# Kernel tuning notes

Measured on AMD Instinct MI355X. Metric: run time of the kernel, lower is better.

## Reference

```python
import jax, jax.numpy as jnp
import numpy as np

B, S, D_MODEL, FFN, P = 8, 4096, 256, 1024, 8
BLK = 256  # token block size for the max-plus reduction


def setup_inputs() -> dict:
    key = jax.random.key(0)
    ks = jax.random.split(key, 12)
    x = jax.random.normal(ks[0], (B, S, D_MODEL), jnp.float32)
    # TropicalLinear params (additive semiring weights -> small scale)
    Wt = 0.05 * jax.random.normal(ks[1], (FFN, D_MODEL), jnp.float32)
    bt = 0.05 * jax.random.normal(ks[2], (FFN,), jnp.float32)
    # LFDualActivation: per-channel piecewise-linear convex (max) and concave (min)
    # branches, blended by a per-channel sigmoid gate alpha ('blend' mode).
    sl_cvx = 1.0 + 0.1 * jax.random.normal(ks[3], (FFN, P), jnp.float32)
    of_cvx = 0.1 * jax.random.normal(ks[4], (FFN, P), jnp.float32)
    sl_ccv = 1.0 + 0.1 * jax.random.normal(ks[5], (FFN, P), jnp.float32)
    of_ccv = 0.1 * jax.random.normal(ks[6], (FFN, P), jnp.float32)
    alpha = jnp.zeros((FFN,), jnp.float32)
    # Classical branch
    Wc = jax.random.normal(ks[7], (D_MODEL, FFN), jnp.float32) / np.sqrt(D_MODEL)
    bc = jnp.zeros((FFN,), jnp.float32)
    # Gate: init per source (weight ~0, bias +2.0 -> g ~ 0.88 tropical)
    Wg = 0.01 * jax.random.normal(ks[8], (D_MODEL, FFN), jnp.float32)
    bg = 2.0 * jnp.ones((FFN,), jnp.float32)
    # Down projection
    Wd = jax.random.normal(ks[9], (FFN, D_MODEL), jnp.float32) / np.sqrt(FFN)
    bd = jnp.zeros((D_MODEL,), jnp.float32)
    return {"x": x, "Wt": Wt, "bt": bt, "sl_cvx": sl_cvx, "of_cvx": of_cvx,
            "sl_ccv": sl_ccv, "of_ccv": of_ccv, "alpha": alpha,
            "Wc": Wc, "bc": bc, "Wg": Wg, "bg": bg, "Wd": Wd, "bd": bd}


def reference(x, Wt, bt, sl_cvx, of_cvx, sl_ccv, of_ccv, alpha, Wc, bc, Wg, bg, Wd, bd):
    Bx, Sx, D = x.shape
    T = Bx * Sx
    xf = x.reshape(T, D)
    xb = xf.reshape(T // BLK, BLK, D)
    s = jax.nn.sigmoid(alpha)  # [FFN]

    def blk_fn(xx):  # xx: [BLK, D]
        # Tropical (max-plus) linear: t[n,m] = max_k(xx[n,k] + Wt[m,k]) + bt[m]
        t = jnp.max(xx[:, None, :] + Wt[None, :, :], axis=-1) + bt  # [BLK, FFN]
        # LF dual activation: blend of convex (max of lines) and concave (min of lines)
        z = t[:, :, None]  # [BLK, FFN, 1]
        cvx = jnp.max(z * sl_cvx[None] + of_cvx[None], axis=-1)
        ccv = jnp.min(z * sl_ccv[None] + of_ccv[None], axis=-1)
        return s * cvx + (1.0 - s) * ccv  # [BLK, FFN]

    trop = jax.lax.map(blk_fn, xb).reshape(T, FFN)  # dropout = identity (eval)
    classical = jax.nn.gelu(xf @ Wc + bc, approximate=False)
    g = jax.nn.sigmoid(xf @ Wg + bg)
    fused = g * trop + (1.0 - g) * classical
    out = fused @ Wd + bd  # final dropout = identity (eval)
    return out.reshape(Bx, Sx, D)
```

## Files before the change

### kernel.cpp

```cpp
#include <hip/hip_runtime.h>

#define TTOK 32768
#define DM   256
#define NF   1024
#define KMAX 32

typedef __attribute__((ext_vector_type(8))) unsigned short ushort8;
typedef __attribute__((ext_vector_type(8))) __bf16 bf16x8;
typedef __attribute__((ext_vector_type(4))) float floatx4;

constexpr size_t O_SLOT = 0;
constexpr size_t O_S    = 256;
constexpr size_t O_WCT  = O_S    + 4096;
constexpr size_t O_WGT  = O_WCT  + (size_t)NF*DM*2;
constexpr size_t O_WDT  = O_WGT  + (size_t)NF*DM*2;
constexpr size_t O_WTT  = O_WDT  + (size_t)DM*NF*2;
constexpr size_t O_XBF  = O_WTT  + (size_t)DM*NF*4;
constexpr size_t O_CNT  = O_XBF  + (size_t)TTOK*DM*2;
constexpr size_t O_CIDX = O_CNT  + (size_t)TTOK*4;
constexpr size_t O_CVAL = O_CIDX + (size_t)TTOK*KMAX*4;
constexpr size_t O_FUSD = O_CVAL + (size_t)TTOK*KMAX*4;

__device__ __forceinline__ float bf2f(unsigned short u) {
    union { unsigned int i; float f; } c; c.i = ((unsigned int)u) << 16; return c.f;
}
__device__ __forceinline__ unsigned short f2bf(float v) {
    union { float f; unsigned int i; } c; c.f = v;
    unsigned int b = c.i;
    return (unsigned short)((b + 0x7FFFu + ((b >> 16) & 1u)) >> 16);
}
__device__ __forceinline__ float sigm(float z) { return 1.0f / (1.0f + __expf(-z)); }
__device__ __forceinline__ float gelu_f(float x) {
    return x * sigm(1.59576912f * (x + 0.044715f * x * x * x));
}
__device__ __forceinline__ void g2lds16(const unsigned short* g, unsigned short* l) {
    __builtin_amdgcn_global_load_lds((const __attribute__((address_space(1))) unsigned int*)g,
                                     (__attribute__((address_space(3))) unsigned int*)l, 16, 0, 0);
}

__global__ void pack_kernel(const float* __restrict__ Wt, const float* __restrict__ alpha,
                            const float* __restrict__ Wc, const float* __restrict__ Wg,
                            const float* __restrict__ Wd,
                            unsigned short* __restrict__ Wct, unsigned short* __restrict__ Wgt,
                            unsigned short* __restrict__ WdT, float* __restrict__ WtT,
                            float* __restrict__ s, unsigned int* __restrict__ slot) {
    int e = blockIdx.x * 256 + threadIdx.x;
    if (e == 0) *slot = 0u;
    { int f = e >> 8, k = e & 255;
      Wct[e] = f2bf(Wc[k * NF + f]);
      Wgt[e] = f2bf(Wg[k * NF + f]); }
    { int n = e >> 10, k = e & 1023;
      WdT[e] = f2bf(Wd[k * DM + n]); }
    { int d = e >> 10, f = e & 1023;
      WtT[e] = Wt[f * DM + d]; }
    if (e < NF) s[e] = sigm(alpha[e]);
}

__global__ void minmax_kernel(const float* __restrict__ Wt, unsigned int* __restrict__ slot) {
    int g = blockIdx.x * 256 + threadIdx.x;
    float lm = 0.0f;
    for (int i = g; i < NF * DM; i += 128 * 256) lm = fmaxf(lm, fabsf(Wt[i]));
    #pragma unroll
    for (int o = 32; o > 0; o >>= 1) lm = fmaxf(lm, __shfl_xor(lm, o));
    if ((threadIdx.x & 63) == 0) atomicMax(slot, __float_as_uint(lm));
}

__global__ __launch_bounds__(256) void cand_kernel(
        const float* __restrict__ x, const unsigned int* __restrict__ slot,
        unsigned short* __restrict__ xbf, int* __restrict__ counts,
        int* __restrict__ cidx, float* __restrict__ cval) {
    const int wave = threadIdx.x >> 6, lane = threadIdx.x & 63;
    const int tok = blockIdx.x * 4 + wave;
    const float* xr = x + (size_t)tok * DM;
    float v0 = xr[lane], v1 = xr[lane + 64], v2 = xr[lane + 128], v3 = xr[lane + 192];
    unsigned short* xo = xbf + (size_t)tok * DM;
    xo[lane]       = f2bf(v0);
    xo[lane + 64]  = f2bf(v1);
    xo[lane + 128] = f2bf(v2);
    xo[lane + 192] = f2bf(v3);
    float m = fmaxf(fmaxf(v0, v1), fmaxf(v2, v3));
    #pragma unroll
    for (int o = 32; o > 0; o >>= 1) m = fmaxf(m, __shfl_xor(m, o));
    const float delta = 2.0f * __uint_as_float(*slot);
    const float thr = m - delta;
    const unsigned long long lt = (lane == 63) ? 0x7FFFFFFFFFFFFFFFull
                                               : ((1ull << lane) - 1ull);
    float vv[4] = { v0, v1, v2, v3 };
    int base = 0;
    #pragma unroll
    for (int j = 0; j < 4; j++) {
        bool p = vv[j] >= thr;
        unsigned long long mask = __ballot(p);
        int pos = base + __popcll(mask & lt);
        if (p && pos < KMAX) {
            cidx[(size_t)tok * KMAX + pos] = lane + j * 64;
            cval[(size_t)tok * KMAX + pos] = vv[j];
        }
        base += __popcll(mask);
    }
    if (lane == 0) counts[tok] = base;
}

#define LDSS  32
#define KCAP  16
#define KPADL 17
#define OSTR  136
#define STAGEB 24576
__global__ __launch_bounds__(512, 4) void gemm1_kernel(
    const unsigned short* __restrict__ A,
    const unsigned short* __restrict__ Bct,
    const unsigned short* __restrict__ Bgt,
    const float* __restrict__ bc, const float* __restrict__ bg,
    const int* __restrict__ counts, const int* __restrict__ cidx,
    const float* __restrict__ cval, const float* __restrict__ x,
    const float* __restrict__ WtT, const float* __restrict__ bt,
    const float* __restrict__ slx, const float* __restrict__ ofx,
    const float* __restrict__ slc, const float* __restrict__ ofc,
    const float* __restrict__ s, unsigned short* __restrict__ fused) {
    __shared__ __align__(16) char smem[76800];
    unsigned short* obuf = (unsigned short*)smem;
    float* par = (float*)(smem + 49152);
    int* sOV  = (int*)(smem + 67584);
    int* sCnt = (int*)(smem + 76288);
    const int t = threadIdx.x;
    const int b = blockIdx.x;
    const int xcd = b & 7, j = b >> 3;
    const int bf = j & 7;
    const int bm = (j >> 3) * 8 + xcd;
    const int wave = t >> 6, lane = t & 63;
    const int wm = wave & 1, wn = wave >> 1;
    const int lr = lane & 15, quad = lane >> 4;
    const int srow = wave * 16 + (lane >> 2), scol = (lane & 3) << 3;
    const unsigned short* gA = A   + (size_t)(bm * 128 + srow) * DM + scol;
    const unsigned short* gC = Bct + (size_t)(bf * 128 + srow) * DM + scol;
    const unsigned short* gG = Bgt + (size_t)(bf * 128 + srow) * DM + scol;
    const int lofs = wave * 16 * LDSS;

    if (t < 128) sCnt[t] = counts[bm * 128 + t];
    const int PADV = (int)(((unsigned int)f2bf(-1e30f)) << 16);
    #pragma unroll
    for (int e = t; e < 2048; e += 512) {
        int m = e >> 4, k = e & 15;
        int c = counts[bm * 128 + m];
        int pk = PADV;
        if (k < (c < KCAP ? c : KCAP)) {
            int d  = cidx[(size_t)(bm * 128 + m) * KMAX + k];
            float v = cval[(size_t)(bm * 128 + m) * KMAX + k];
            pk = (int)(((unsigned int)f2bf(v)) << 16) | d;
        }
        sOV[m * KPADL + k] = pk;
    }
    #pragma unroll
    for (int e = t; e < 1024; e += 512) {
        int ff = e >> 3, w = e & 7;
        int gf = (bf * 128 + ff) * 8 + w;
        par[ff * 36 + w]      = slx[gf];
        par[ff * 36 + 8 + w]  = ofx[gf];
        par[ff * 36 + 16 + w] = slc[gf];
        par[ff * 36 + 24 + w] = ofc[gf];
    }
    if (t < 128) {
        int gf = bf * 128 + t;
        par[t * 36 + 32] = bt[gf];
        par[t * 36 + 33] = s[gf];
        par[t * 36 + 34] = bc[gf];
        par[t * 36 + 35] = bg[gf];
    }

    floatx4 accc[4][2], accg[4][2];
    #pragma unroll
    for (int i = 0; i < 4; i++)
        #pragma unroll
        for (int jj = 0; jj < 2; jj++) { accc[i][jj] = (floatx4)0.0f; accg[i][jj] = (floatx4)0.0f; }

    {
        unsigned short* b0 = (unsigned short*)smem;
        g2lds16(gA, b0 + lofs);
        g2lds16(gC, b0 + 4096 + lofs);
        g2lds16(gG, b0 + 8192 + lofs);
    }
    __syncthreads();
    #pragma unroll
    for (int k = 0; k < 8; k++) {
        unsigned short* cur = (unsigned short*)(smem + (size_t)(k & 1) * STAGEB);
        if (k < 7) {
            unsigned short* nxt = (unsigned short*)(smem + (size_t)((k + 1) & 1) * STAGEB);
            int k0 = (k + 1) * 32;
            g2lds16(gA + k0, nxt + lofs);
            g2lds16(gC + k0, nxt + 4096 + lofs);
            g2lds16(gG + k0, nxt + 8192 + lofs);
        }
        bf16x8 af[4], bcf[2], bgf[2];
        #pragma unroll
        for (int mi = 0; mi < 4; mi++)
            af[mi] = *(const bf16x8*)&cur[(wm * 64 + mi * 16 + lr) * LDSS + quad * 8];
        #pragma unroll
        for (int ni = 0; ni < 2; ni++) {
            bcf[ni] = *(const bf16x8*)&cur[4096 + (wn * 32 + ni * 16 + lr) * LDSS + quad * 8];
            bgf[ni] = *(const bf16x8*)&cur[8192 + (wn * 32 + ni * 16 + lr) * LDSS + quad * 8];
        }
        #pragma unroll
        for (int mi = 0; mi < 4; mi++)
            #pragma unroll
            for (int ni = 0; ni < 2; ni++) {
                accc[mi][ni] = __builtin_amdgcn_mfma_f32_16x16x32_bf16(af[mi], bcf[ni], accc[mi][ni], 0, 0, 0);
                accg[mi][ni] = __builtin_amdgcn_mfma_f32_16x16x32_bf16(af[mi], bgf[ni], accg[mi][ni], 0, 0, 0);
            }
        __syncthreads();
    }

    const int f0 = bf * 128 + wn * 32 + lr;
    #pragma unroll
    for (int mi = 0; mi < 4; mi++) {
        const int mb = wm * 64 + mi * 16 + quad * 4;
        int c0 = sCnt[mb], c1 = sCnt[mb + 1], c2 = sCnt[mb + 2], c3 = sCnt[mb + 3];
        int k0c = c0 < KCAP ? c0 : KCAP, k1c = c1 < KCAP ? c1 : KCAP;
        int k2c = c2 < KCAP ? c2 : KCAP, k3c = c3 < KCAP ? c3 : KCAP;
        int km = max(max(k0c, k1c), max(k2c, k3c));
        float z0a = -1e30f, z1a = -1e30f, z2a = -1e30f, z3a = -1e30f;
        float z0b = -1e30f, z1b = -1e30f, z2b = -1e30f, z3b = -1e30f;
        for (int k = 0; k < km; k++) {
            int p0 = sOV[(mb + 0) * KPADL + k];
            int p1 = sOV[(mb + 1) * KPADL + k];
            int p2 = sOV[(mb + 2) * KPADL + k];
            int p3 = sOV[(mb + 3) * KPADL + k];
            const float* r0 = WtT + ((p0 & 0xFFFF) << 10) + f0;
            const float* r1 = WtT + ((p1 & 0xFFFF) << 10) + f0;
            const float* r2 = WtT + ((p2 & 0xFFFF) << 10) + f0;
            const float* r3 = WtT + ((p3 & 0xFFFF) << 10) + f0;
            float w0a = r0[0], w0b = r0[16];
            float w1a = r1[0], w1b = r1[16];
            float w2a = r2[0], w2b = r2[16];
            float w3a = r3[0], w3b = r3[16];
            float v0 = __int_as_float(p0 & 0xFFFF0000);
            float v1 = __int_as_float(p1 & 0xFFFF0000);
            float v2 = __int_as_float(p2 & 0xFFFF0000);
            float v3 = __int_as_float(p3 & 0xFFFF0000);
            z0a = fmaxf(z0a, v0 + w0a); z0b = fmaxf(z0b, v0 + w0b);
            z1a = fmaxf(z1a, v1 + w1a); z1b = fmaxf(z1b, v1 + w1b);
            z2a = fmaxf(z2a, v2 + w2a); z2b = fmaxf(z2b, v2 + w2b);
            z3a = fmaxf(z3a, v3 + w3a); z3b = fmaxf(z3b, v3 + w3b);
        }
        if (c0 > KCAP || c1 > KCAP || c2 > KCAP || c3 > KCAP) {
            float za[4] = { z0a, z1a, z2a, z3a };
            float zb[4] = { z0b, z1b, z2b, z3b };
            int cc[4] = { c0, c1, c2, c3 };
            #pragma unroll 1
            for (int r = 0; r < 4; r++) if (cc[r] > KCAP) {
                const float* xr = x + (size_t)(bm * 128 + mb + r) * DM;
                float ma = -1e30f, mbv = -1e30f;
                for (int d = 0; d < DM; d++) {
                    float xv = xr[d];
                    ma  = fmaxf(ma,  xv + WtT[d * NF + f0]);
                    mbv = fmaxf(mbv, xv + WtT[d * NF + f0 + 16]);
                }
                za[r] = ma; zb[r] = mbv;
            }
            z0a = za[0]; z1a = za[1]; z2a = za[2]; z3a = za[3];
            z0b = zb[0]; z1b = zb[1]; z2b = zb[2]; z3b = zb[3];
        }
        #pragma unroll
        for (int ni = 0; ni < 2; ni++) {
            const int fl = wn * 32 + ni * 16 + lr;
            const float* pp = par + fl * 36;
            float4 a0 = *(const float4*)(pp),      a1 = *(const float4*)(pp + 4);
            float4 b0 = *(const float4*)(pp + 8),  b1 = *(const float4*)(pp + 12);
            float4 cc0 = *(const float4*)(pp + 16), cc1 = *(const float4*)(pp + 20);
            float4 d0 = *(const float4*)(pp + 24), d1 = *(const float4*)(pp + 28);
            float4 sc = *(const float4*)(pp + 32);
            float zr[4];
            if (ni == 0) { zr[0] = z0a; zr[1] = z1a; zr[2] = z2a; zr[3] = z3a; }
            else         { zr[0] = z0b; zr[1] = z1b; zr[2] = z2b; zr[3] = z3b; }
            #pragma unroll
            for (int r = 0; r < 4; r++) {
                float z = zr[r] + sc.x;
                float cvx = fmaf(z, a0.x, b0.x);
                cvx = fmaxf(cvx, fmaf(z, a0.y, b0.y));
                cvx = fmaxf(cvx, fmaf(z, a0.z, b0.z));
                cvx = fmaxf(cvx, fmaf(z, a0.w, b0.w));
                cvx = fmaxf(cvx, fmaf(z, a1.x, b1.x));
                cvx = fmaxf(cvx, fmaf(z, a1.y, b1.y));
                cvx = fmaxf(cvx, fmaf(z, a1.z, b1.z));
                cvx = fmaxf(cvx, fmaf(z, a1.w, b1.w));
                float ccv = fmaf(z, cc0.x, d0.x);
                ccv = fminf(ccv, fmaf(z, cc0.y, d0.y));
                ccv = fminf(ccv, fmaf(z, cc0.z, d0.z));
                ccv = fminf(ccv, fmaf(z, cc0.w, d0.w));
                ccv = fminf(ccv, fmaf(z, cc1.x, d1.x));
                ccv = fminf(ccv, fmaf(z, cc1.y, d1.y));
                ccv = fminf(ccv, fmaf(z, cc1.z, d1.z));
                ccv = fminf(ccv, fmaf(z, cc1.w, d1.w));
                float tv = sc.y * cvx + (1.0f - sc.y) * ccv;
                float cpre = accc[mi][ni][r] + sc.z;
                float gpre = accg[mi][ni][r] + sc.w;
                float g = sigm(gpre);
                float cla = gelu_f(cpre);
                obuf[(mb + r) * OSTR + fl] = f2bf(g * tv + (1.0f - g) * cla);
            }
        }
    }
    __syncthreads();
    #pragma unroll
    for (int e = t; e < 128 * 16; e += 512) {
        int row = e >> 4, c8 = (e & 15) << 3;
        ushort8 v = *(const ushort8*)&obuf[row * OSTR + c8];
        *(ushort8*)&fused[(size_t)(bm * 128 + row) * NF + bf * 128 + c8] = v;
    }
}

#define LDS2 64
__global__ __launch_bounds__(512, 4) void gemm2_kernel(
    const unsigned short* __restrict__ A,
    const unsigned short* __restrict__ Bt,
    const float* __restrict__ bd, float* __restrict__ out) {
    __shared__ __align__(16) unsigned short As[128 * LDS2];
    __shared__ __align__(16) unsigned short Bs[128 * LDS2];
    const int t = threadIdx.x;
    const int b = blockIdx.x;
    const int xcd = b & 7, j = b >> 3;
    const int bn = j & 1;
    const int bm = (j >> 1) * 8 + xcd;
    const int wave = t >> 6, lane = t & 63;
    const int wm = wave & 1, wn = wave >> 1;
    const int lr = lane & 15, quad = lane >> 4;
    const int srow = wave * 8 + (lane >> 3), scol = (lane & 7) << 3;
    const unsigned short* gA = A  + (size_t)(bm * 128 + srow) * NF + scol;
    const unsigned short* gB = Bt + (size_t)(bn * 128 + srow) * NF + scol;
    unsigned short* lA = &As[wave * 8 * LDS2];
    unsigned short* lB = &Bs[wave * 8 * LDS2];

    floatx4 acc[4][2];
    #pragma unroll
    for (int i = 0; i < 4; i++)
        #pragma unroll
        for (int jj = 0; jj < 2; jj++) acc[i][jj] = (floatx4)0.0f;

    for (int k0 = 0; k0 < NF; k0 += 64) {
        __syncthreads();
        g2lds16(gA + k0, lA);
        g2lds16(gA + k0 + (size_t)64 * NF, lA + 64 * LDS2);
        g2lds16(gB + k0, lB);
        g2lds16(gB + k0 + (size_t)64 * NF, lB + 64 * LDS2);
        __syncthreads();
        #pragma unroll
        for (int ks = 0; ks < 2; ks++) {
            bf16x8 af[4], bf_[2];
            #pragma unroll
            for (int mi = 0; mi < 4; mi++)
                af[mi] = *(const bf16x8*)&As[(wm * 64 + mi * 16 + lr) * LDS2 + ks * 32 + quad * 8];
            #pragma unroll
            for (int ni = 0; ni < 2; ni++)
                bf_[ni] = *(const bf16x8*)&Bs[(wn * 32 + ni * 16 + lr) * LDS2 + ks * 32 + quad * 8];
            #pragma unroll
            for (int mi = 0; mi < 4; mi++)
                #pragma unroll
                for (int ni = 0; ni < 2; ni++)
                    acc[mi][ni] = __builtin_amdgcn_mfma_f32_16x16x32_bf16(af[mi], bf_[ni], acc[mi][ni], 0, 0, 0);
        }
    }
    #pragma unroll
    for (int mi = 0; mi < 4; mi++)
        #pragma unroll
        for (int ni = 0; ni < 2; ni++) {
            int n = bn * 128 + wn * 32 + ni * 16 + lr;
            float bdv = bd[n];
            #pragma unroll
            for (int r = 0; r < 4; r++) {
                int m = bm * 128 + wm * 64 + mi * 16 + quad * 4 + r;
                out[m * DM + n] = acc[mi][ni][r] + bdv;
            }
        }
}

extern "C" void kernel_launch(void* const* d_in, const int* in_sizes, int n_in,
                              void* d_out, int out_size, void* d_ws, size_t ws_size,
                              hipStream_t stream) {
    const float* x     = (const float*)d_in[0];
    const float* Wt    = (const float*)d_in[1];
    const float* bt    = (const float*)d_in[2];
    const float* slx   = (const float*)d_in[3];
    const float* ofx   = (const float*)d_in[4];
    const float* slc   = (const float*)d_in[5];
    const float* ofc   = (const float*)d_in[6];
    const float* alpha = (const float*)d_in[7];
    const float* Wc    = (const float*)d_in[8];
    const float* bc    = (const float*)d_in[9];
    const float* Wg    = (const float*)d_in[10];
    const float* bg    = (const float*)d_in[11];
    const float* Wd    = (const float*)d_in[12];
    const float* bd    = (const float*)d_in[13];
    float* out = (float*)d_out;
    char* ws = (char*)d_ws;

    unsigned int* slot = (unsigned int*)(ws + O_SLOT);
    float* s           = (float*)(ws + O_S);
    unsigned short* Wct = (unsigned short*)(ws + O_WCT);
    unsigned short* Wgt = (unsigned short*)(ws + O_WGT);
    unsigned short* WdT = (unsigned short*)(ws + O_WDT);
    float* WtT          = (float*)(ws + O_WTT);
    unsigned short* xbf = (unsigned short*)(ws + O_XBF);
    int* counts         = (int*)(ws + O_CNT);
    int* cidx           = (int*)(ws + O_CIDX);
    float* cval         = (float*)(ws + O_CVAL);
    unsigned short* fused = (unsigned short*)(ws + O_FUSD);

    pack_kernel<<<1024, 256, 0, stream>>>(Wt, alpha, Wc, Wg, Wd, Wct, Wgt, WdT, WtT, s, slot);
    minmax_kernel<<<128, 256, 0, stream>>>(Wt, slot);
    cand_kernel<<<TTOK / 4, 256, 0, stream>>>(x, slot, xbf, counts, cidx, cval);
    gemm1_kernel<<<2048, 512, 0, stream>>>(
        xbf, Wct, Wgt, bc, bg, counts, cidx, cval, x, WtT, bt,
        slx, ofx, slc, ofc, s, fused);
    gemm2_kernel<<<512, 512, 0, stream>>>(fused, WdT, bd, out);
}
```

Measured before the change: 328.5 us.

## Fuse Wt max into pack, defer gemm1 prologue, double-buffer gemm2, pack epilogue math

The separate minmax kernel is removed. Its |Wt| max reduction now runs inside pack_kernel, and the slot is zeroed with a memset. In gemm1, staging of candidates and activation parameters moves after the MFMA main loop so it no longer delays the first tile loads, and the final barrier is dropped. gemm2 moves from single-buffered LDS with two barriers per step to double-buffered prefetch. The max-plus gather and dual-activation epilogue are rewritten with 2-wide float vectors so the compiler can emit packed FMA/max/min. Together these cut a launch, overlap loads with MFMA, and reduce epilogue instruction count, at the cost of more LDS in gemm2 (which may lower occupancy).

```diff
diff --git a/kernel.cpp b/kernel.cpp
--- a/kernel.cpp
+++ b/kernel.cpp
@@ -8,6 +8,11 @@
 typedef __attribute__((ext_vector_type(8))) unsigned short ushort8;
 typedef __attribute__((ext_vector_type(8))) __bf16 bf16x8;
 typedef __attribute__((ext_vector_type(4))) float floatx4;
+typedef __attribute__((ext_vector_type(2))) float floatx2;
+
+#define PKFMA(a,b,c) __builtin_elementwise_fma(a,b,c)
+#define PKMAX(a,b)   __builtin_elementwise_max(a,b)
+#define PKMIN(a,b)   __builtin_elementwise_min(a,b)
 
 constexpr size_t O_SLOT = 0;
 constexpr size_t O_S    = 256;
@@ -45,24 +50,20 @@
                             unsigned short* __restrict__ WdT, float* __restrict__ WtT,
                             float* __restrict__ s, unsigned int* __restrict__ slot) {
     int e = blockIdx.x * 256 + threadIdx.x;
-    if (e == 0) *slot = 0u;
     { int f = e >> 8, k = e & 255;
       Wct[e] = f2bf(Wc[k * NF + f]);
       Wgt[e] = f2bf(Wg[k * NF + f]); }
     { int n = e >> 10, k = e & 1023;
       WdT[e] = f2bf(Wd[k * DM + n]); }
+    float wv;
     { int d = e >> 10, f = e & 1023;
-      WtT[e] = Wt[f * DM + d]; }
-    if (e < NF) s[e] = sigm(alpha[e]);
-}
-
-__global__ void minmax_kernel(const float* __restrict__ Wt, unsigned int* __restrict__ slot) {
-    int g = blockIdx.x * 256 + threadIdx.x;
-    float lm = 0.0f;
-    for (int i = g; i < NF * DM; i += 128 * 256) lm = fmaxf(lm, fabsf(Wt[i]));
+      wv = Wt[f * DM + d];
+      WtT[e] = wv; }
+    float lm = fabsf(wv);
     #pragma unroll
     for (int o = 32; o > 0; o >>= 1) lm = fmaxf(lm, __shfl_xor(lm, o));
     if ((threadIdx.x & 63) == 0) atomicMax(slot, __float_as_uint(lm));
+    if (e < NF) s[e] = sigm(alpha[e]);
 }
 
 __global__ __launch_bounds__(256) void cand_kernel(
@@ -137,35 +138,6 @@
     const int lofs = wave * 16 * LDSS;
 
     if (t < 128) sCnt[t] = counts[bm * 128 + t];
-    const int PADV = (int)(((unsigned int)f2bf(-1e30f)) << 16);
-    #pragma unroll
-    for (int e = t; e < 2048; e += 512) {
-        int m = e >> 4, k = e & 15;
-        int c = counts[bm * 128 + m];
-        int pk = PADV;
-        if (k < (c < KCAP ? c : KCAP)) {
-            int d  = cidx[(size_t)(bm * 128 + m) * KMAX + k];
-            float v = cval[(size_t)(bm * 128 + m) * KMAX + k];
-            pk = (int)(((unsigned int)f2bf(v)) << 16) | d;
-        }
-        sOV[m * KPADL + k] = pk;
-    }
-    #pragma unroll
-    for (int e = t; e < 1024; e += 512) {
-        int ff = e >> 3, w = e & 7;
-        int gf = (bf * 128 + ff) * 8 + w;
-        par[ff * 36 + w]      = slx[gf];
-        par[ff * 36 + 8 + w]  = ofx[gf];
-        par[ff * 36 + 16 + w] = slc[gf];
-        par[ff * 36 + 24 + w] = ofc[gf];
-    }
-    if (t < 128) {
-        int gf = bf * 128 + t;
-        par[t * 36 + 32] = bt[gf];
-        par[t * 36 + 33] = s[gf];
-        par[t * 36 + 34] = bc[gf];
-        par[t * 36 + 35] = bg[gf];
-    }
 
     floatx4 accc[4][2], accg[4][2];
     #pragma unroll
@@ -206,8 +178,37 @@
                 accc[mi][ni] = __builtin_amdgcn_mfma_f32_16x16x32_bf16(af[mi], bcf[ni], accc[mi][ni], 0, 0, 0);
                 accg[mi][ni] = __builtin_amdgcn_mfma_f32_16x16x32_bf16(af[mi], bgf[ni], accg[mi][ni], 0, 0, 0);
             }
-        __syncthreads();
-    }
+        if (k < 7) __syncthreads();
+    }
+
+    const int PADV = (int)(((unsigned int)f2bf(-1e30f)) << 16);
+    for (int e = t; e < 2048; e += 512) {
+        int m = e >> 4, k = e & 15;
+        int c = sCnt[m];
+        int pk = PADV;
+        if (k < (c < KCAP ? c : KCAP)) {
+            int d  = cidx[(size_t)(bm * 128 + m) * KMAX + k];
+            float v = cval[(size_t)(bm * 128 + m) * KMAX + k];
+            pk = (int)(((unsigned int)f2bf(v)) << 16) | d;
+        }
+        sOV[m * KPADL + k] = pk;
+    }
+    for (int e = t; e < 1024; e += 512) {
+        int ff = e >> 3, w = e & 7;
+        int gf = (bf * 128 + ff) * 8 + w;
+        par[ff * 36 + w]      = slx[gf];
+        par[ff * 36 + 8 + w]  = ofx[gf];
+        par[ff * 36 + 16 + w] = slc[gf];
+        par[ff * 36 + 24 + w] = ofc[gf];
+    }
+    if (t < 128) {
+        int gf = bf * 128 + t;
+        par[t * 36 + 32] = bt[gf];
+        par[t * 36 + 33] = s[gf];
+        par[t * 36 + 34] = bc[gf];
+        par[t * 36 + 35] = bg[gf];
+    }
+    __syncthreads();
 
     const int f0 = bf * 128 + wn * 32 + lr;
     #pragma unroll
@@ -217,8 +218,7 @@
         int k0c = c0 < KCAP ? c0 : KCAP, k1c = c1 < KCAP ? c1 : KCAP;
         int k2c = c2 < KCAP ? c2 : KCAP, k3c = c3 < KCAP ? c3 : KCAP;
         int km = max(max(k0c, k1c), max(k2c, k3c));
-        float z0a = -1e30f, z1a = -1e30f, z2a = -1e30f, z3a = -1e30f;
-        float z0b = -1e30f, z1b = -1e30f, z2b = -1e30f, z3b = -1e30f;
+        floatx2 zp0 = { -1e30f, -1e30f }, zp1 = zp0, zp2 = zp0, zp3 = zp0;
         for (int k = 0; k < km; k++) {
             int p0 = sOV[(mb + 0) * KPADL + k];
             int p1 = sOV[(mb + 1) * KPADL + k];
@@ -228,22 +228,23 @@
             const float* r1 = WtT + ((p1 & 0xFFFF) << 10) + f0;
             const float* r2 = WtT + ((p2 & 0xFFFF) << 10) + f0;
             const float* r3 = WtT + ((p3 & 0xFFFF) << 10) + f0;
-            float w0a = r0[0], w0b = r0[16];
-            float w1a = r1[0], w1b = r1[16];
-            float w2a = r2[0], w2b = r2[16];
-            float w3a = r3[0], w3b = r3[16];
-            float v0 = __int_as_float(p0 & 0xFFFF0000);
-            float v1 = __int_as_float(p1 & 0xFFFF0000);
-            float v2 = __int_as_float(p2 & 0xFFFF0000);
-            float v3 = __int_as_float(p3 & 0xFFFF0000);
-            z0a = fmaxf(z0a, v0 + w0a); z0b = fmaxf(z0b, v0 + w0b);
-            z1a = fmaxf(z1a, v1 + w1a); z1b = fmaxf(z1b, v1 + w1b);
-            z2a = fmaxf(z2a, v2 + w2a); z2b = fmaxf(z2b, v2 + w2b);
-            z3a = fmaxf(z3a, v3 + w3a); z3b = fmaxf(z3b, v3 + w3b);
+            floatx2 w0 = { r0[0], r0[16] };
+            floatx2 w1 = { r1[0], r1[16] };
+            floatx2 w2 = { r2[0], r2[16] };
+            floatx2 w3 = { r3[0], r3[16] };
+            float s0 = __int_as_float(p0 & 0xFFFF0000);
+            float s1 = __int_as_float(p1 & 0xFFFF0000);
+            float s2 = __int_as_float(p2 & 0xFFFF0000);
+            float s3 = __int_as_float(p3 & 0xFFFF0000);
+            floatx2 v0 = { s0, s0 }, v1 = { s1, s1 }, v2 = { s2, s2 }, v3 = { s3, s3 };
+            zp0 = PKMAX(zp0, v0 + w0);
+            zp1 = PKMAX(zp1, v1 + w1);
+            zp2 = PKMAX(zp2, v2 + w2);
+            zp3 = PKMAX(zp3, v3 + w3);
         }
         if (c0 > KCAP || c1 > KCAP || c2 > KCAP || c3 > KCAP) {
-            float za[4] = { z0a, z1a, z2a, z3a };
-            float zb[4] = { z0b, z1b, z2b, z3b };
+            float za[4] = { zp0.x, zp1.x, zp2.x, zp3.x };
+            float zb[4] = { zp0.y, zp1.y, zp2.y, zp3.y };
             int cc[4] = { c0, c1, c2, c3 };
             #pragma unroll 1
             for (int r = 0; r < 4; r++) if (cc[r] > KCAP) {
@@ -256,9 +257,11 @@
                 }
                 za[r] = ma; zb[r] = mbv;
             }
-            z0a = za[0]; z1a = za[1]; z2a = za[2]; z3a = za[3];
-            z0b = zb[0]; z1b = zb[1]; z2b = zb[2]; z3b = zb[3];
-        }
+            zp0.x = za[0]; zp1.x = za[1]; zp2.x = za[2]; zp3.x = za[3];
+            zp0.y = zb[0]; zp1.y = zb[1]; zp2.y = zb[2]; zp3.y = zb[3];
+        }
+        float z0a = zp0.x, z0b = zp0.y, z1a = zp1.x, z1b = zp1.y;
+        float z2a = zp2.x, z2b = zp2.y, z3a = zp3.x, z3b = zp3.y;
         #pragma unroll
         for (int ni = 0; ni < 2; ni++) {
             const int fl = wn * 32 + ni * 16 + lr;
@@ -268,28 +271,27 @@
             float4 cc0 = *(const float4*)(pp + 16), cc1 = *(const float4*)(pp + 20);
             float4 d0 = *(const float4*)(pp + 24), d1 = *(const float4*)(pp + 28);
             float4 sc = *(const float4*)(pp + 32);
+            floatx2 sA0 = { a0.x, a0.y }, sA1 = { a0.z, a0.w };
+            floatx2 sA2 = { a1.x, a1.y }, sA3 = { a1.z, a1.w };
+            floatx2 oA0 = { b0.x, b0.y }, oA1 = { b0.z, b0.w };
+            floatx2 oA2 = { b1.x, b1.y }, oA3 = { b1.z, b1.w };
+            floatx2 sC0 = { cc0.x, cc0.y }, sC1 = { cc0.z, cc0.w };
+            floatx2 sC2 = { cc1.x, cc1.y }, sC3 = { cc1.z, cc1.w };
+            floatx2 oC0 = { d0.x, d0.y }, oC1 = { d0.z, d0.w };
+            floatx2 oC2 = { d1.x, d1.y }, oC3 = { d1.z, d1.w };
             float zr[4];
             if (ni == 0) { zr[0] = z0a; zr[1] = z1a; zr[2] = z2a; zr[3] = z3a; }
             else         { zr[0] = z0b; zr[1] = z1b; zr[2] = z2b; zr[3] = z3b; }
             #pragma unroll
             for (int r = 0; r < 4; r++) {
-                float z = zr[r] + sc.x;
-                float cvx = fmaf(z, a0.x, b0.x);
-                cvx = fmaxf(cvx, fmaf(z, a0.y, b0.y));
-                cvx = fmaxf(cvx, fmaf(z, a0.z, b0.z));
-                cvx = fmaxf(cvx, fmaf(z, a0.w, b0.w));
-                cvx = fmaxf(cvx, fmaf(z, a1.x, b1.x));
-                cvx = fmaxf(cvx, fmaf(z, a1.y, b1.y));
-                cvx = fmaxf(cvx, fmaf(z, a1.z, b1.z));
-                cvx = fmaxf(cvx, fmaf(z, a1.w, b1.w));
-                float ccv = fmaf(z, cc0.x, d0.x);
-                ccv = fminf(ccv, fmaf(z, cc0.y, d0.y));
-                ccv = fminf(ccv, fmaf(z, cc0.z, d0.z));
-                ccv = fminf(ccv, fmaf(z, cc0.w, d0.w));
-                ccv = fminf(ccv, fmaf(z, cc1.x, d1.x));
-                ccv = fminf(ccv, fmaf(z, cc1.y, d1.y));
-                ccv = fminf(ccv, fmaf(z, cc1.z, d1.z));
-                ccv = fminf(ccv, fmaf(z, cc1.w, d1.w));
+                float zv = zr[r] + sc.x;
+                floatx2 zz = { zv, zv };
+                floatx2 tx = PKMAX(PKMAX(PKFMA(zz, sA0, oA0), PKFMA(zz, sA1, oA1)),
+                                   PKMAX(PKFMA(zz, sA2, oA2), PKFMA(zz, sA3, oA3)));
+                float cvx = fmaxf(tx.x, tx.y);
+                floatx2 tn = PKMIN(PKMIN(PKFMA(zz, sC0, oC0), PKFMA(zz, sC1, oC1)),
+                                   PKMIN(PKFMA(zz, sC2, oC2), PKFMA(zz, sC3, oC3)));
+                float ccv = fminf(tn.x, tn.y);
                 float tv = sc.y * cvx + (1.0f - sc.y) * ccv;
                 float cpre = accc[mi][ni][r] + sc.z;
                 float gpre = accg[mi][ni][r] + sc.w;
@@ -309,12 +311,12 @@
 }
 
 #define LDS2 64
+#define S2B  32768
 __global__ __launch_bounds__(512, 4) void gemm2_kernel(
     const unsigned short* __restrict__ A,
     const unsigned short* __restrict__ Bt,
     const float* __restrict__ bd, float* __restrict__ out) {
-    __shared__ __align__(16) unsigned short As[128 * LDS2];
-    __shared__ __align__(16) unsigned short Bs[128 * LDS2];
+    __shared__ __align__(16) char smem[65536];
     const int t = threadIdx.x;
     const int b = blockIdx.x;
     const int xcd = b & 7, j = b >> 3;
@@ -326,8 +328,7 @@
     const int srow = wave * 8 + (lane >> 3), scol = (lane & 7) << 3;
     const unsigned short* gA = A  + (size_t)(bm * 128 + srow) * NF + scol;
     const unsigned short* gB = Bt + (size_t)(bn * 128 + srow) * NF + scol;
-    unsigned short* lA = &As[wave * 8 * LDS2];
-    unsigned short* lB = &Bs[wave * 8 * LDS2];
+    const int lofs = wave * 8 * LDS2;
 
     floatx4 acc[4][2];
     #pragma unroll
@@ -335,28 +336,41 @@
         #pragma unroll
         for (int jj = 0; jj < 2; jj++) acc[i][jj] = (floatx4)0.0f;
 
-    for (int k0 = 0; k0 < NF; k0 += 64) {
-        __syncthreads();
-        g2lds16(gA + k0, lA);
-        g2lds16(gA + k0 + (size_t)64 * NF, lA + 64 * LDS2);
-        g2lds16(gB + k0, lB);
-        g2lds16(gB + k0 + (size_t)64 * NF, lB + 64 * LDS2);
-        __syncthreads();
+    {
+        unsigned short* b0 = (unsigned short*)smem;
+        g2lds16(gA, b0 + lofs);
+        g2lds16(gA + (size_t)64 * NF, b0 + 64 * LDS2 + lofs);
+        g2lds16(gB, b0 + 8192 + lofs);
+        g2lds16(gB + (size_t)64 * NF, b0 + 8192 + 64 * LDS2 + lofs);
+    }
+    __syncthreads();
+    #pragma unroll
+    for (int k = 0; k < 16; k++) {
+        unsigned short* cur = (unsigned short*)(smem + (size_t)(k & 1) * S2B);
+        if (k < 15) {
+            unsigned short* nxt = (unsigned short*)(smem + (size_t)((k + 1) & 1) * S2B);
+            int k0 = (k + 1) * 64;
+            g2lds16(gA + k0, nxt + lofs);
+            g2lds16(gA + k0 + (size_t)64 * NF, nxt + 64 * LDS2 + lofs);
+            g2lds16(gB + k0, nxt + 8192 + lofs);
+            g2lds16(gB + k0 + (size_t)64 * NF, nxt + 8192 + 64 * LDS2 + lofs);
+        }
         #pragma unroll
         for (int ks = 0; ks < 2; ks++) {
             bf16x8 af[4], bf_[2];
             #pragma unroll
             for (int mi = 0; mi < 4; mi++)
-                af[mi] = *(const bf16x8*)&As[(wm * 64 + mi * 16 + lr) * LDS2 + ks * 32 + quad * 8];
+                af[mi] = *(const bf16x8*)&cur[(wm * 64 + mi * 16 + lr) * LDS2 + ks * 32 + quad * 8];
             #pragma unroll
             for (int ni = 0; ni < 2; ni++)
-                bf_[ni] = *(const bf16x8*)&Bs[(wn * 32 + ni * 16 + lr) * LDS2 + ks * 32 + quad * 8];
+                bf_[ni] = *(const bf16x8*)&cur[8192 + (wn * 32 + ni * 16 + lr) * LDS2 + ks * 32 + quad * 8];
             #pragma unroll
             for (int mi = 0; mi < 4; mi++)
                 #pragma unroll
                 for (int ni = 0; ni < 2; ni++)
                     acc[mi][ni] = __builtin_amdgcn_mfma_f32_16x16x32_bf16(af[mi], bf_[ni], acc[mi][ni], 0, 0, 0);
         }
+        if (k < 15) __syncthreads();
     }
     #pragma unroll
     for (int mi = 0; mi < 4; mi++)
@@ -404,8 +418,8 @@
     float* cval         = (float*)(ws + O_CVAL);
     unsigned short* fused = (unsigned short*)(ws + O_FUSD);
 
+    hipMemsetAsync(slot, 0, 4, stream);
     pack_kernel<<<1024, 256, 0, stream>>>(Wt, alpha, Wc, Wg, Wd, Wct, Wgt, WdT, WtT, s, slot);
-    minmax_kernel<<<128, 256, 0, stream>>>(Wt, slot);
     cand_kernel<<<TTOK / 4, 256, 0, stream>>>(x, slot, xbf, counts, cidx, cval);
     gemm1_kernel<<<2048, 512, 0, stream>>>(
         xbf, Wct, Wgt, bc, bg, counts, cidx, cval, x, WtT, bt,
```

Result: slower. 354.3 us (+7.9%).
